# Kernel tuning notes

Measured on AMD Instinct MI355X. Metric: run time of the kernel, lower is better.

The kernel has to match this reference:

```python
import jax, jax.numpy as jnp
import numpy as np

SEQ, EMBED, H, QLR, KVLR, RD, VD = 4096, 2048, 16, 512, 512, 64, 128
KD = VD + RD  # full key/query head dim (content + rope)


def _make_rotary_pe(seq_len, dim):
    inv_freq = 1.0 / jnp.power(10000.0, jnp.arange(0, dim, 2) / dim)
    t = jnp.arange(seq_len)
    freqs = jnp.outer(t, inv_freq)  # (seq, dim//2)
    return jnp.sin(freqs), jnp.cos(freqs)


def _apply_rope(x, sin, cos):
    # x: (seq, ..., dim); sin/cos: (seq, dim//2)
    d = x.shape[-1] // 2
    x1, x2 = x[..., :d], x[..., d:]
    sin2 = jnp.concatenate([sin, sin], axis=-1)
    cos2 = jnp.concatenate([cos, cos], axis=-1)
    ne = x.ndim - 2
    sin2 = sin2.reshape(sin2.shape[0], *[1] * ne, sin2.shape[1])
    cos2 = cos2.reshape(cos2.shape[0], *[1] * ne, cos2.shape[1])
    rot = jnp.concatenate([-x2, x1], axis=-1)
    return x * cos2 + rot * sin2


def setup_inputs() -> dict:
    key = jax.random.key(0)
    ks = jax.random.split(key, 8)

    def w(k, out_dim, in_dim):
        return jax.random.normal(k, (out_dim, in_dim), dtype=jnp.float32) * (1.0 / np.sqrt(in_dim))

    x = jax.random.normal(ks[0], (SEQ, EMBED), dtype=jnp.float32)
    mask = jnp.tril(jnp.ones((SEQ, SEQ), dtype=bool))  # causal
    return {
        "x": x,
        "mask": mask,
        "w_q_down": w(ks[1], QLR, EMBED),
        "w_q_up": w(ks[2], H * VD, QLR),
        "w_q_rope": w(ks[3], H * RD, QLR),
        "w_kv_down": w(ks[4], KVLR, EMBED),
        "w_kv_up": w(ks[5], H * 2 * VD, KVLR),
        "w_k_rope": w(ks[6], RD, EMBED),
        "w_out": w(ks[7], EMBED, H * VD),
    }


def reference(x, mask, w_q_down, w_q_up, w_q_rope, w_kv_down, w_kv_up, w_k_rope, w_out):
    seq = x.shape[0]
    # query path through low-rank bottleneck
    c_q = x @ w_q_down.T                                   # (S, QLR)
    q_content = (c_q @ w_q_up.T).reshape(seq, H, VD)       # (S, H, VD)
    q_rope = (c_q @ w_q_rope.T).reshape(seq, H, RD)        # (S, H, RD)
    # kv path through shared low-rank bottleneck
    c_kv = x @ w_kv_down.T                                 # (S, KVLR)
    kv = c_kv @ w_kv_up.T                                  # (S, H*2*VD)
    k_content_flat, v_flat = jnp.split(kv, 2, axis=-1)
    k_content = k_content_flat.reshape(seq, H, VD)
    v = v_flat.reshape(seq, H, VD)
    # shared rope key (one per token, broadcast to heads)
    k_rope_shared = (x @ w_k_rope.T)[:, None, :]           # (S, 1, RD)
    sin, cos = _make_rotary_pe(seq, RD)
    q_rope_rot = _apply_rope(q_rope, sin, cos)             # (S, H, RD)
    k_rope_rot = jnp.tile(_apply_rope(k_rope_shared, sin, cos), (1, H, 1))
    q_final = jnp.concatenate([q_content, q_rope_rot], axis=-1)  # (S, H, KD)
    k_final = jnp.concatenate([k_content, k_rope_rot], axis=-1)  # (S, H, KD)
    # values zero-padded to key dim
    v_padded = jnp.concatenate(
        [v, jnp.zeros((seq, H, RD), dtype=v.dtype)], axis=-1)    # (S, H, KD)
    # scaled dot-product attention per head
    scale = 1.0 / jnp.sqrt(jnp.asarray(KD, dtype=x.dtype))
    scores = jnp.einsum("shd,thd->hst", q_final, k_final) * scale  # (H, S, S)
    scores = jnp.where(mask[None, :, :], scores, jnp.asarray(-1e9, dtype=scores.dtype))
    probs = jax.nn.softmax(scores, axis=-1)
    attn = jnp.einsum("hst,thd->shd", probs, v_padded)             # (S, H, KD)
    attn = attn[..., :VD].reshape(seq, H * VD)                     # drop zero-pad dims
    return attn @ w_out.T                                          # (S, EMBED)
```

## Files before the change

### kernel.cpp

```cpp
#include <hip/hip_runtime.h>


#define SEQ   4096
#define EMBED 2048
#define NHEAD 16
#define QLR   512
#define KVLR  512
#define RD    64
#define VD    128
#define KDIM  192

#define QSCALE 0.104121521f

typedef __attribute__((ext_vector_type(8)))  _Float16 half8;
typedef __attribute__((ext_vector_type(4)))  _Float16 half4;
typedef __attribute__((ext_vector_type(4)))  float    f32x4;
typedef __attribute__((ext_vector_type(16))) float    f32x16;
typedef __attribute__((ext_vector_type(2)))  unsigned int uint2v;
typedef __attribute__((ext_vector_type(4)))  unsigned int uint4v;

__device__ __forceinline__ void gload16(void* lds, const void* g) {
    __builtin_amdgcn_global_load_lds(
        (const __attribute__((address_space(1))) void*)g,
        (__attribute__((address_space(3))) void*)lds, 16, 0, 0);
}

__device__ __forceinline__ unsigned int pkh(float a, float b) {
    auto h = __builtin_amdgcn_cvt_pkrtz(a, b);
    return __builtin_bit_cast(unsigned int, h);
}

__global__ __launch_bounds__(256) void cvt_plain(const float* __restrict__ s,
                                                 _Float16* __restrict__ d, int n8) {
    const int i = blockIdx.x * 256 + threadIdx.x;
    if (i >= n8) return;
    const float4 a = reinterpret_cast<const float4*>(s)[i * 2];
    const float4 b = reinterpret_cast<const float4*>(s)[i * 2 + 1];
    half8 r;
    r[0] = (_Float16)a.x; r[1] = (_Float16)a.y; r[2] = (_Float16)a.z; r[3] = (_Float16)a.w;
    r[4] = (_Float16)b.x; r[5] = (_Float16)b.y; r[6] = (_Float16)b.z; r[7] = (_Float16)b.w;
    reinterpret_cast<half8*>(d)[i] = r;
}

__global__ __launch_bounds__(256) void cvt_down(const float* __restrict__ wqd,
                                                const float* __restrict__ wkvd,
                                                const float* __restrict__ wkr,
                                                _Float16* __restrict__ dst) {
    const int i = blockIdx.x * 256 + threadIdx.x;
    if (i >= 1152 * 2048 / 8) return;
    const int e = i * 8, row = e >> 11, col = e & 2047;
    const float* src = row < 512  ? wqd  + (size_t)row * 2048 + col
                     : row < 1024 ? wkvd + (size_t)(row - 512) * 2048 + col
                     : row < 1088 ? wkr  + (size_t)(row - 1024) * 2048 + col
                                  : nullptr;
    half8 r = {};
    if (src) {
        const float4 a = reinterpret_cast<const float4*>(src)[0];
        const float4 b = reinterpret_cast<const float4*>(src)[1];
        r[0] = (_Float16)a.x; r[1] = (_Float16)a.y; r[2] = (_Float16)a.z; r[3] = (_Float16)a.w;
        r[4] = (_Float16)b.x; r[5] = (_Float16)b.y; r[6] = (_Float16)b.z; r[7] = (_Float16)b.w;
    }
    reinterpret_cast<half8*>(dst)[i] = r;
}

__global__ __launch_bounds__(256) void cvt_qup(const float* __restrict__ wqu,
                                               const float* __restrict__ wqr,
                                               _Float16* __restrict__ dst) {
    const int i = blockIdx.x * 256 + threadIdx.x;
    if (i >= 3072 * 512 / 8) return;
    const int e = i * 8, row = e >> 9, col = e & 511;
    const float* src = row < 2048 ? wqu + (size_t)row * 512 + col
                                  : wqr + (size_t)(row - 2048) * 512 + col;
    const float4 a = reinterpret_cast<const float4*>(src)[0];
    const float4 b = reinterpret_cast<const float4*>(src)[1];
    half8 r;
    r[0] = (_Float16)a.x; r[1] = (_Float16)a.y; r[2] = (_Float16)a.z; r[3] = (_Float16)a.w;
    r[4] = (_Float16)b.x; r[5] = (_Float16)b.y; r[6] = (_Float16)b.z; r[7] = (_Float16)b.w;
    reinterpret_cast<half8*>(dst)[i] = r;
}

template <int EPI>
__global__ __launch_bounds__(256) void gemm_f16(const _Float16* __restrict__ A,
                                                const _Float16* __restrict__ B,
                                                _Float16* __restrict__ o0,
                                                _Float16* __restrict__ o1,
                                                _Float16* __restrict__ o2,
                                                float* __restrict__ of,
                                                int M, int N, int K)
{
    __shared__ _Float16 sA[128 * 64];
    __shared__ _Float16 sB[128 * 64];

    const int tid  = threadIdx.x;
    const int wid  = tid >> 6;
    const int lane = tid & 63;
    const int lr   = lane & 15;
    const int lg   = lane >> 4;
    const int row0 = blockIdx.y * 128;
    const int col0 = blockIdx.x * 128;
    const int war  = (wid >> 1) * 64;
    const int wac  = (wid & 1) * 64;

    const int sr = lane >> 3;
    const int sk = (lane & 7) * 8;
    const _Float16* Ab = A + (size_t)(row0 + wid * 8 + sr) * K + sk;
    const _Float16* Bb = B + (size_t)(col0 + wid * 8 + sr) * K + sk;

    f32x4 acc[4][4] = {};

    for (int k0 = 0; k0 < K; k0 += 64) {
#pragma unroll
        for (int i = 0; i < 4; ++i) {
            const int c = i * 4 + wid;
            gload16((char*)sA + c * 1024, Ab + (size_t)i * 32 * K + k0);
            gload16((char*)sB + c * 1024, Bb + (size_t)i * 32 * K + k0);
        }
        __syncthreads();

#pragma unroll
        for (int kk = 0; kk < 64; kk += 32) {
            half8 a[4], b[4];
#pragma unroll
            for (int i = 0; i < 4; ++i)
                a[i] = *reinterpret_cast<const half8*>(&sA[(war + i * 16 + lr) * 64 + kk + lg * 8]);
#pragma unroll
            for (int j = 0; j < 4; ++j)
                b[j] = *reinterpret_cast<const half8*>(&sB[(wac + j * 16 + lr) * 64 + kk + lg * 8]);
            __builtin_amdgcn_s_setprio(1);
#pragma unroll
            for (int i = 0; i < 4; ++i)
#pragma unroll
                for (int j = 0; j < 4; ++j)
                    acc[i][j] = __builtin_amdgcn_mfma_f32_16x16x32_f16(a[i], b[j], acc[i][j], 0, 0, 0);
            __builtin_amdgcn_s_setprio(0);
        }
        __syncthreads();
    }

#pragma unroll
    for (int i = 0; i < 4; ++i)
#pragma unroll
        for (int j = 0; j < 4; ++j) {
            const int grow0 = row0 + war + i * 16 + lg * 4;
            const int gcol  = col0 + wac + j * 16 + lr;
            if constexpr (EPI == 2) {
                if (gcol >= 2048) {
                    half4 pv;
#pragma unroll
                    for (int r = 0; r < 4; ++r) pv[r] = (_Float16)acc[i][j][r];
                    *reinterpret_cast<half4*>(&o1[(size_t)(gcol - 2048) * SEQ + grow0]) = pv;
                    continue;
                }
            }
#pragma unroll
            for (int r = 0; r < 4; ++r) {
                const int grow = grow0 + r;
                const float v = acc[i][j][r];
                if constexpr (EPI == 0) {
                    if (gcol < 512)       o0[(size_t)grow * 512 + gcol] = (_Float16)v;
                    else if (gcol < 1024) o1[(size_t)grow * 512 + gcol - 512] = (_Float16)v;
                    else if (gcol < 1088) o2[(size_t)grow * 64 + gcol - 1024] = (_Float16)v;
                } else if constexpr (EPI == 1) {
                    const float vs = v * QSCALE;
                    if (gcol < 2048)
                        o0[(size_t)grow * (NHEAD * KDIM) + (gcol >> 7) * KDIM + (gcol & 127)] = (_Float16)vs;
                    else {
                        const int c = gcol - 2048;
                        o0[(size_t)grow * (NHEAD * KDIM) + (c >> 6) * KDIM + VD + (c & 63)] = (_Float16)vs;
                    }
                } else if constexpr (EPI == 2) {
                    o0[((size_t)(gcol >> 7) * SEQ + grow) * KDIM + (gcol & 127)] = (_Float16)v;
                } else {
                    of[(size_t)grow * N + gcol] = v;
                }
            }
        }
}

__global__ __launch_bounds__(256) void rope_kernel(_Float16* __restrict__ qf,
                                                   _Float16* __restrict__ kf,
                                                   const _Float16* __restrict__ ktmp)
{
    __shared__ float s_sin[32], s_cos[32];
    const int s   = blockIdx.x;
    const int tid = threadIdx.x;
    if (tid < 32) {
        const double inv = exp(-(double)tid * (log(10000.0) / 32.0));
        const double ang = (double)s * inv;
        s_sin[tid] = (float)sin(ang);
        s_cos[tid] = (float)cos(ang);
    }
    __syncthreads();

    for (int p = tid; p < NHEAD * 32; p += 256) {
        const int h = p >> 5, i = p & 31;
        const size_t base = (size_t)s * (NHEAD * KDIM) + h * KDIM + VD;
        const float x1 = (float)qf[base + i];
        const float x2 = (float)qf[base + 32 + i];
        const float cs = s_cos[i], sn = s_sin[i];
        qf[base + i]      = (_Float16)(x1 * cs - x2 * sn);
        qf[base + 32 + i] = (_Float16)(x2 * cs + x1 * sn);
    }
    if (tid < 32) {
        const int i = tid;
        const float x1 = (float)ktmp[(size_t)s * RD + i];
        const float x2 = (float)ktmp[(size_t)s * RD + 32 + i];
        const float cs = s_cos[i], sn = s_sin[i];
        const _Float16 r1 = (_Float16)(x1 * cs - x2 * sn);
        const _Float16 r2 = (_Float16)(x2 * cs + x1 * sn);
#pragma unroll
        for (int h = 0; h < NHEAD; ++h) {
            const size_t base = ((size_t)h * SEQ + s) * KDIM + VD;
            kf[base + i]      = r1;
            kf[base + 32 + i] = r2;
        }
    }
}

__global__ __launch_bounds__(256, 2) void fattn(const _Float16* __restrict__ qf,
                                                const _Float16* __restrict__ kf,
                                                const _Float16* __restrict__ vT,
                                                _Float16* __restrict__ attn)
{
    __shared__ _Float16 sK[2][64 * 192];
    __shared__ _Float16 sV[2][128 * 64];

    const int idx = blockIdx.x;
    const int h   = idx & 15;
    const int qt  = 31 - (idx >> 4);
    const int q0  = qt * 128;

    const int tid  = threadIdx.x;
    const int wid  = tid >> 6;
    const int lane = tid & 63;
    const int l31  = lane & 31;
    const int h5   = lane >> 5;
    const int x7   = l31 & 7;
    const int qg   = q0 + wid * 32 + l31;
    const int q0w  = q0 + wid * 32;

    const _Float16* ksrc[6];
    int klds[6];
#pragma unroll
    for (int i = 0; i < 6; ++i) {
        const int c   = wid * 6 + i;
        const int gi  = c * 64 + lane;
        const int row = gi / 24;
        const int g   = gi % 24;
        ksrc[i] = kf + ((size_t)h * SEQ + row) * KDIM + ((g ^ (row & 7)) << 3);
        klds[i] = c * 1024;
    }
    const _Float16* vsrc[4];
    int vlds[4];
#pragma unroll
    for (int i = 0; i < 4; ++i) {
        const int c = wid * 4 + i;
        const int d = c * 8 + (lane >> 3);
        vsrc[i] = vT + ((size_t)h * VD + d) * SEQ + (((lane & 7) ^ (lane >> 3)) << 3);
        vlds[i] = c * 1024;
    }

    half8 qfr[12];
    {
        const _Float16* qb_ = qf + (size_t)qg * (NHEAD * KDIM) + h * KDIM + h5 * 8;
#pragma unroll
        for (int ks = 0; ks < 12; ++ks)
            qfr[ks] = *reinterpret_cast<const half8*>(qb_ + ks * 16);
    }

    f32x16 o0 = {}, o1 = {}, o2 = {}, o3 = {};
    float m_ = -1e30f, l_ = 0.0f;

    const int nt = 2 * qt + 2;

#pragma unroll
    for (int i = 0; i < 6; ++i) gload16((char*)sK[0] + klds[i], ksrc[i]);
#pragma unroll
    for (int i = 0; i < 4; ++i) gload16((char*)sV[0] + vlds[i], vsrc[i]);
    __syncthreads();

    int cur = 0;
    for (int t = 0; t < nt; ++t) {
        const int j0 = t * 64;

        if (t + 1 < nt) {
            const size_t joff = (size_t)(j0 + 64) * KDIM;
#pragma unroll
            for (int i = 0; i < 6; ++i)
                gload16((char*)sK[cur ^ 1] + klds[i], ksrc[i] + joff);
#pragma unroll
            for (int i = 0; i < 4; ++i)
                gload16((char*)sV[cur ^ 1] + vlds[i], vsrc[i] + j0 + 64);
        }

        f32x16 s0 = {}, s1 = {};
        {
            const char* kb = (const char*)sK[cur];
            __builtin_amdgcn_s_setprio(1);
#pragma unroll
            for (int ks = 0; ks < 12; ++ks) {
                const int go = ((ks * 2 + h5) ^ x7) << 4;
                const half8 ka = *reinterpret_cast<const half8*>(kb + l31 * 384 + go);
                const half8 kc = *reinterpret_cast<const half8*>(kb + (32 + l31) * 384 + go);
                s0 = __builtin_amdgcn_mfma_f32_32x32x16_f16(ka, qfr[ks], s0, 0, 0, 0);
                s1 = __builtin_amdgcn_mfma_f32_32x32x16_f16(kc, qfr[ks], s1, 0, 0, 0);
            }
            __builtin_amdgcn_s_setprio(0);
        }

        if (j0 + 63 > q0w) {
#pragma unroll
            for (int m = 0; m < 16; ++m) {
                const int kv = j0 + (m & 3) + 8 * (m >> 2) + 4 * h5;
                if (kv > qg)      s0[m] = -3.0e38f;
                if (kv + 32 > qg) s1[m] = -3.0e38f;
            }
        }

        float ma = fmaxf(s0[0], s0[1]);
        float mb = fmaxf(s1[0], s1[1]);
#pragma unroll
        for (int m = 2; m < 16; m += 2) {
            ma = fmaxf(fmaxf(ma, s0[m]), s0[m + 1]);
            mb = fmaxf(fmaxf(mb, s1[m]), s1[m + 1]);
        }
        float mx = fmaxf(ma, mb);
        mx = fmaxf(mx, __shfl_xor(mx, 32, 64));

        if (!__all(mx - m_ <= 11.5f)) {
            const float mn = fmaxf(m_, mx);
            const float alpha = exp2f(m_ - mn);
            m_ = mn;
            l_ *= alpha;
#pragma unroll
            for (int m = 0; m < 16; ++m) {
                o0[m] *= alpha; o1[m] *= alpha; o2[m] *= alpha; o3[m] *= alpha;
            }
        }
        float ra = 0.0f, rb = 0.0f, rc = 0.0f, rd = 0.0f;
#pragma unroll
        for (int m = 0; m < 16; m += 2) {
            const float pa = exp2f(s0[m] - m_);     s0[m] = pa;     ra += pa;
            const float pc = exp2f(s0[m + 1] - m_); s0[m + 1] = pc; rb += pc;
            const float pe = exp2f(s1[m] - m_);     s1[m] = pe;     rc += pe;
            const float pg = exp2f(s1[m + 1] - m_); s1[m + 1] = pg; rd += pg;
        }
        float rs = (ra + rb) + (rc + rd);
        rs += __shfl_xor(rs, 32, 64);
        l_ += rs;

        half8 pb0, pb1, pb2, pb3;
        {
            unsigned int x, x2, y, y2;
            x  = pkh(s0[0], s0[1]);  x2 = pkh(s0[2], s0[3]);
            y  = pkh(s0[4], s0[5]);  y2 = pkh(s0[6], s0[7]);
            uint2v r1 = __builtin_amdgcn_permlane32_swap(x, y, false, false);
            uint2v r2 = __builtin_amdgcn_permlane32_swap(x2, y2, false, false);
            { uint4v u = { r1[0], r2[0], r1[1], r2[1] }; pb0 = __builtin_bit_cast(half8, u); }
            x  = pkh(s0[8], s0[9]);  x2 = pkh(s0[10], s0[11]);
            y  = pkh(s0[12], s0[13]); y2 = pkh(s0[14], s0[15]);
            r1 = __builtin_amdgcn_permlane32_swap(x, y, false, false);
            r2 = __builtin_amdgcn_permlane32_swap(x2, y2, false, false);
            { uint4v u = { r1[0], r2[0], r1[1], r2[1] }; pb1 = __builtin_bit_cast(half8, u); }
            x  = pkh(s1[0], s1[1]);  x2 = pkh(s1[2], s1[3]);
            y  = pkh(s1[4], s1[5]);  y2 = pkh(s1[6], s1[7]);
            r1 = __builtin_amdgcn_permlane32_swap(x, y, false, false);
            r2 = __builtin_amdgcn_permlane32_swap(x2, y2, false, false);
            { uint4v u = { r1[0], r2[0], r1[1], r2[1] }; pb2 = __builtin_bit_cast(half8, u); }
            x  = pkh(s1[8], s1[9]);  x2 = pkh(s1[10], s1[11]);
            y  = pkh(s1[12], s1[13]); y2 = pkh(s1[14], s1[15]);
            r1 = __builtin_amdgcn_permlane32_swap(x, y, false, false);
            r2 = __builtin_amdgcn_permlane32_swap(x2, y2, false, false);
            { uint4v u = { r1[0], r2[0], r1[1], r2[1] }; pb3 = __builtin_bit_cast(half8, u); }
        }

        {
            const char* vbse = (const char*)sV[cur];
            __builtin_amdgcn_s_setprio(1);
#pragma unroll
            for (int ks = 0; ks < 4; ++ks) {
                const int go = ((ks * 2 + h5) ^ x7) << 4;
                const half8 pbk = ks == 0 ? pb0 : ks == 1 ? pb1 : ks == 2 ? pb2 : pb3;
                const half8 v0 = *reinterpret_cast<const half8*>(vbse + (l31)      * 128 + go);
                const half8 v1 = *reinterpret_cast<const half8*>(vbse + (32 + l31) * 128 + go);
                const half8 v2 = *reinterpret_cast<const half8*>(vbse + (64 + l31) * 128 + go);
                const half8 v3 = *reinterpret_cast<const half8*>(vbse + (96 + l31) * 128 + go);
                o0 = __builtin_amdgcn_mfma_f32_32x32x16_f16(v0, pbk, o0, 0, 0, 0);
                o1 = __builtin_amdgcn_mfma_f32_32x32x16_f16(v1, pbk, o1, 0, 0, 0);
                o2 = __builtin_amdgcn_mfma_f32_32x32x16_f16(v2, pbk, o2, 0, 0, 0);
                o3 = __builtin_amdgcn_mfma_f32_32x32x16_f16(v3, pbk, o3, 0, 0, 0);
            }
            __builtin_amdgcn_s_setprio(0);
        }

        __syncthreads();
        cur ^= 1;
    }

    const float invl = 1.0f / l_;
    _Float16* ob = attn + (size_t)qg * (NHEAD * VD) + h * VD + 4 * h5;
#pragma unroll
    for (int g = 0; g < 4; ++g) {
#pragma unroll
        for (int pp = 0; pp < 2; ++pp) {
            const int m = g * 4 + pp * 2;
            const int dof = pp * 2 + 8 * g;
            *reinterpret_cast<unsigned int*>(ob + dof) =
                pkh(o0[m] * invl, o0[m + 1] * invl);
            *reinterpret_cast<unsigned int*>(ob + 32 + dof) =
                pkh(o1[m] * invl, o1[m + 1] * invl);
            *reinterpret_cast<unsigned int*>(ob + 64 + dof) =
                pkh(o2[m] * invl, o2[m + 1] * invl);
            *reinterpret_cast<unsigned int*>(ob + 96 + dof) =
                pkh(o3[m] * invl, o3[m + 1] * invl);
        }
    }
}

extern "C" void kernel_launch(void* const* d_in, const int* in_sizes, int n_in,
                              void* d_out, int out_size, void* d_ws, size_t ws_size,
                              hipStream_t stream)
{
    (void)in_sizes; (void)n_in; (void)out_size; (void)ws_size;
    const float* x    = (const float*)d_in[0];
    const float* wqd  = (const float*)d_in[2];
    const float* wqu  = (const float*)d_in[3];
    const float* wqr  = (const float*)d_in[4];
    const float* wkvd = (const float*)d_in[5];
    const float* wkvu = (const float*)d_in[6];
    const float* wkr  = (const float*)d_in[7];
    const float* wout = (const float*)d_in[8];
    float* out = (float*)d_out;

    char* ws = (char*)d_ws;
    _Float16* x_h    = (_Float16*)ws; ws += (size_t)SEQ * EMBED * 2;
    _Float16* wdownh = (_Float16*)ws; ws += (size_t)1152 * EMBED * 2;
    _Float16* wquph  = (_Float16*)ws; ws += (size_t)3072 * QLR * 2;
    _Float16* wkvuh  = (_Float16*)ws; ws += (size_t)4096 * KVLR * 2;
    _Float16* c_q    = (_Float16*)ws; ws += (size_t)SEQ * QLR * 2;
    _Float16* c_kv   = (_Float16*)ws; ws += (size_t)SEQ * KVLR * 2;
    _Float16* ktmp   = (_Float16*)ws; ws += (size_t)SEQ * RD * 2;
    _Float16* qfin   = (_Float16*)ws; ws += (size_t)SEQ * NHEAD * KDIM * 2;
    _Float16* kfin   = (_Float16*)ws; ws += (size_t)SEQ * NHEAD * KDIM * 2;
    _Float16* vT     = (_Float16*)ws; ws += (size_t)NHEAD * VD * SEQ * 2;
    _Float16* attn   = x_h;
    _Float16* wouth  = c_q;

    dim3 blk(256);

    cvt_plain<<<dim3(4096), blk, 0, stream>>>(x, x_h, SEQ * EMBED / 8);
    cvt_down <<<dim3(1152), blk, 0, stream>>>(wqd, wkvd, wkr, wdownh);
    cvt_qup  <<<dim3(768),  blk, 0, stream>>>(wqu, wqr, wquph);
    cvt_plain<<<dim3(1024), blk, 0, stream>>>(wkvu, wkvuh, 4096 * KVLR / 8);

    gemm_f16<0><<<dim3(9, 32), blk, 0, stream>>>(
        x_h, wdownh, c_q, c_kv, ktmp, nullptr, SEQ, 1152, EMBED);
    gemm_f16<1><<<dim3(24, 32), blk, 0, stream>>>(
        c_q, wquph, qfin, nullptr, nullptr, nullptr, SEQ, 3072, QLR);
    gemm_f16<2><<<dim3(32, 32), blk, 0, stream>>>(
        c_kv, wkvuh, kfin, vT, nullptr, nullptr, SEQ, 4096, KVLR);

    cvt_plain<<<dim3(2048), blk, 0, stream>>>(wout, wouth, EMBED * EMBED / 8);

    rope_kernel<<<dim3(SEQ), blk, 0, stream>>>(qfin, kfin, ktmp);
    fattn<<<dim3(512), blk, 0, stream>>>(qfin, kfin, vT, attn);
    gemm_f16<3><<<dim3(16, 32), blk, 0, stream>>>(
        attn, wouth, nullptr, nullptr, nullptr, out, SEQ, EMBED, NHEAD * VD);
}
```

Baseline: 346.9 us.

## Give each attention wave two query sub-tiles to reuse K/V fragments

```diff
diff --git a/kernel.cpp b/kernel.cpp
--- a/kernel.cpp
+++ b/kernel.cpp
@@ -28,6 +28,14 @@
 __device__ __forceinline__ unsigned int pkh(float a, float b) {
     auto h = __builtin_amdgcn_cvt_pkrtz(a, b);
     return __builtin_bit_cast(unsigned int, h);
+}
+
+__device__ __forceinline__ float fexp2(float x) {
+#if __has_builtin(__builtin_amdgcn_exp2f)
+    return __builtin_amdgcn_exp2f(x);
+#else
+    return exp2f(x);
+#endif
 }
 
 __global__ __launch_bounds__(256) void cvt_plain(const float* __restrict__ s,
@@ -217,188 +225,82 @@
     }
 }
 
-__global__ __launch_bounds__(256, 2) void fattn(const _Float16* __restrict__ qf,
-                                                const _Float16* __restrict__ kf,
-                                                const _Float16* __restrict__ vT,
-                                                _Float16* __restrict__ attn)
+__device__ __forceinline__ void sm_pack(f32x16& s0, f32x16& s1,
+                                        f32x16& o0, f32x16& o1,
+                                        f32x16& o2, f32x16& o3,
+                                        float& m_, float& l_,
+                                        int j0, int qg, int q0base, int h5,
+                                        half8& pb0, half8& pb1,
+                                        half8& pb2, half8& pb3)
 {
-    __shared__ _Float16 sK[2][64 * 192];
-    __shared__ _Float16 sV[2][128 * 64];
-
-    const int idx = blockIdx.x;
-    const int h   = idx & 15;
-    const int qt  = 31 - (idx >> 4);
-    const int q0  = qt * 128;
-
-    const int tid  = threadIdx.x;
-    const int wid  = tid >> 6;
-    const int lane = tid & 63;
-    const int l31  = lane & 31;
-    const int h5   = lane >> 5;
-    const int x7   = l31 & 7;
-    const int qg   = q0 + wid * 32 + l31;
-    const int q0w  = q0 + wid * 32;
-
-    const _Float16* ksrc[6];
-    int klds[6];
-#pragma unroll
-    for (int i = 0; i < 6; ++i) {
-        const int c   = wid * 6 + i;
-        const int gi  = c * 64 + lane;
-        const int row = gi / 24;
-        const int g   = gi % 24;
-        ksrc[i] = kf + ((size_t)h * SEQ + row) * KDIM + ((g ^ (row & 7)) << 3);
-        klds[i] = c * 1024;
-    }
-    const _Float16* vsrc[4];
-    int vlds[4];
-#pragma unroll
-    for (int i = 0; i < 4; ++i) {
-        const int c = wid * 4 + i;
-        const int d = c * 8 + (lane >> 3);
-        vsrc[i] = vT + ((size_t)h * VD + d) * SEQ + (((lane & 7) ^ (lane >> 3)) << 3);
-        vlds[i] = c * 1024;
-    }
-
-    half8 qfr[12];
-    {
-        const _Float16* qb_ = qf + (size_t)qg * (NHEAD * KDIM) + h * KDIM + h5 * 8;
-#pragma unroll
-        for (int ks = 0; ks < 12; ++ks)
-            qfr[ks] = *reinterpret_cast<const half8*>(qb_ + ks * 16);
-    }
-
-    f32x16 o0 = {}, o1 = {}, o2 = {}, o3 = {};
-    float m_ = -1e30f, l_ = 0.0f;
-
-    const int nt = 2 * qt + 2;
-
-#pragma unroll
-    for (int i = 0; i < 6; ++i) gload16((char*)sK[0] + klds[i], ksrc[i]);
-#pragma unroll
-    for (int i = 0; i < 4; ++i) gload16((char*)sV[0] + vlds[i], vsrc[i]);
-    __syncthreads();
-
-    int cur = 0;
-    for (int t = 0; t < nt; ++t) {
-        const int j0 = t * 64;
-
-        if (t + 1 < nt) {
-            const size_t joff = (size_t)(j0 + 64) * KDIM;
-#pragma unroll
-            for (int i = 0; i < 6; ++i)
-                gload16((char*)sK[cur ^ 1] + klds[i], ksrc[i] + joff);
-#pragma unroll
-            for (int i = 0; i < 4; ++i)
-                gload16((char*)sV[cur ^ 1] + vlds[i], vsrc[i] + j0 + 64);
-        }
-
-        f32x16 s0 = {}, s1 = {};
-        {
-            const char* kb = (const char*)sK[cur];
-            __builtin_amdgcn_s_setprio(1);
-#pragma unroll
-            for (int ks = 0; ks < 12; ++ks) {
-                const int go = ((ks * 2 + h5) ^ x7) << 4;
-                const half8 ka = *reinterpret_cast<const half8*>(kb + l31 * 384 + go);
-                const half8 kc = *reinterpret_cast<const half8*>(kb + (32 + l31) * 384 + go);
-                s0 = __builtin_amdgcn_mfma_f32_32x32x16_f16(ka, qfr[ks], s0, 0, 0, 0);
-                s1 = __builtin_amdgcn_mfma_f32_32x32x16_f16(kc, qfr[ks], s1, 0, 0, 0);
-            }
-            __builtin_amdgcn_s_setprio(0);
-        }
-
-        if (j0 + 63 > q0w) {
-#pragma unroll
-            for (int m = 0; m < 16; ++m) {
-                const int kv = j0 + (m & 3) + 8 * (m >> 2) + 4 * h5;
-                if (kv > qg)      s0[m] = -3.0e38f;
-                if (kv + 32 > qg) s1[m] = -3.0e38f;
-            }
-        }
-
-        float ma = fmaxf(s0[0], s0[1]);
-        float mb = fmaxf(s1[0], s1[1]);
-#pragma unroll
-        for (int m = 2; m < 16; m += 2) {
-            ma = fmaxf(fmaxf(ma, s0[m]), s0[m + 1]);
-            mb = fmaxf(fmaxf(mb, s1[m]), s1[m + 1]);
-        }
-        float mx = fmaxf(ma, mb);
-        mx = fmaxf(mx, __shfl_xor(mx, 32, 64));
-
-        if (!__all(mx - m_ <= 11.5f)) {
-            const float mn = fmaxf(m_, mx);
-            const float alpha = exp2f(m_ - mn);
-            m_ = mn;
-            l_ *= alpha;
-#pragma unroll
-            for (int m = 0; m < 16; ++m) {
-                o0[m] *= alpha; o1[m] *= alpha; o2[m] *= alpha; o3[m] *= alpha;
-            }
-        }
-        float ra = 0.0f, rb = 0.0f, rc = 0.0f, rd = 0.0f;
-#pragma unroll
-        for (int m = 0; m < 16; m += 2) {
-            const float pa = exp2f(s0[m] - m_);     s0[m] = pa;     ra += pa;
-            const float pc = exp2f(s0[m + 1] - m_); s0[m + 1] = pc; rb += pc;
-            const float pe = exp2f(s1[m] - m_);     s1[m] = pe;     rc += pe;
-            const float pg = exp2f(s1[m + 1] - m_); s1[m + 1] = pg; rd += pg;
-        }
-        float rs = (ra + rb) + (rc + rd);
-        rs += __shfl_xor(rs, 32, 64);
-        l_ += rs;
-
-        half8 pb0, pb1, pb2, pb3;
-        {
-            unsigned int x, x2, y, y2;
-            x  = pkh(s0[0], s0[1]);  x2 = pkh(s0[2], s0[3]);
-            y  = pkh(s0[4], s0[5]);  y2 = pkh(s0[6], s0[7]);
-            uint2v r1 = __builtin_amdgcn_permlane32_swap(x, y, false, false);
-            uint2v r2 = __builtin_amdgcn_permlane32_swap(x2, y2, false, false);
-            { uint4v u = { r1[0], r2[0], r1[1], r2[1] }; pb0 = __builtin_bit_cast(half8, u); }
-            x  = pkh(s0[8], s0[9]);  x2 = pkh(s0[10], s0[11]);
-            y  = pkh(s0[12], s0[13]); y2 = pkh(s0[14], s0[15]);
-            r1 = __builtin_amdgcn_permlane32_swap(x, y, false, false);
-            r2 = __builtin_amdgcn_permlane32_swap(x2, y2, false, false);
-            { uint4v u = { r1[0], r2[0], r1[1], r2[1] }; pb1 = __builtin_bit_cast(half8, u); }
-            x  = pkh(s1[0], s1[1]);  x2 = pkh(s1[2], s1[3]);
-            y  = pkh(s1[4], s1[5]);  y2 = pkh(s1[6], s1[7]);
-            r1 = __builtin_amdgcn_permlane32_swap(x, y, false, false);
-            r2 = __builtin_amdgcn_permlane32_swap(x2, y2, false, false);
-            { uint4v u = { r1[0], r2[0], r1[1], r2[1] }; pb2 = __builtin_bit_cast(half8, u); }
-            x  = pkh(s1[8], s1[9]);  x2 = pkh(s1[10], s1[11]);
-            y  = pkh(s1[12], s1[13]); y2 = pkh(s1[14], s1[15]);
-            r1 = __builtin_amdgcn_permlane32_swap(x, y, false, false);
-            r2 = __builtin_amdgcn_permlane32_swap(x2, y2, false, false);
-            { uint4v u = { r1[0], r2[0], r1[1], r2[1] }; pb3 = __builtin_bit_cast(half8, u); }
-        }
-
-        {
-            const char* vbse = (const char*)sV[cur];
-            __builtin_amdgcn_s_setprio(1);
-#pragma unroll
-            for (int ks = 0; ks < 4; ++ks) {
-                const int go = ((ks * 2 + h5) ^ x7) << 4;
-                const half8 pbk = ks == 0 ? pb0 : ks == 1 ? pb1 : ks == 2 ? pb2 : pb3;
-                const half8 v0 = *reinterpret_cast<const half8*>(vbse + (l31)      * 128 + go);
-                const half8 v1 = *reinterpret_cast<const half8*>(vbse + (32 + l31) * 128 + go);
-                const half8 v2 = *reinterpret_cast<const half8*>(vbse + (64 + l31) * 128 + go);
-                const half8 v3 = *reinterpret_cast<const half8*>(vbse + (96 + l31) * 128 + go);
-                o0 = __builtin_amdgcn_mfma_f32_32x32x16_f16(v0, pbk, o0, 0, 0, 0);
-                o1 = __builtin_amdgcn_mfma_f32_32x32x16_f16(v1, pbk, o1, 0, 0, 0);
-                o2 = __builtin_amdgcn_mfma_f32_32x32x16_f16(v2, pbk, o2, 0, 0, 0);
-                o3 = __builtin_amdgcn_mfma_f32_32x32x16_f16(v3, pbk, o3, 0, 0, 0);
-            }
-            __builtin_amdgcn_s_setprio(0);
-        }
-
-        __syncthreads();
-        cur ^= 1;
-    }
-
+    if (j0 + 63 > q0base) {
+#pragma unroll
+        for (int m = 0; m < 16; ++m) {
+            const int kv = j0 + (m & 3) + 8 * (m >> 2) + 4 * h5;
+            if (kv > qg)      s0[m] = -3.0e38f;
+            if (kv + 32 > qg) s1[m] = -3.0e38f;
+        }
+    }
+    float ma = fmaxf(s0[0], s0[1]);
+    float mb = fmaxf(s1[0], s1[1]);
+#pragma unroll
+    for (int m = 2; m < 16; m += 2) {
+        ma = fmaxf(fmaxf(ma, s0[m]), s0[m + 1]);
+        mb = fmaxf(fmaxf(mb, s1[m]), s1[m + 1]);
+    }
+    float mx = fmaxf(ma, mb);
+    mx = fmaxf(mx, __shfl_xor(mx, 32, 64));
+
+    if (!__all(mx - m_ <= 11.5f)) {
+        const float mn = fmaxf(m_, mx);
+        const float alpha = fexp2(m_ - mn);
+        m_ = mn;
+        l_ *= alpha;
+#pragma unroll
+        for (int m = 0; m < 16; ++m) {
+            o0[m] *= alpha; o1[m] *= alpha; o2[m] *= alpha; o3[m] *= alpha;
+        }
+    }
+    float ra = 0.0f, rb = 0.0f, rc = 0.0f, rd = 0.0f;
+#pragma unroll
+    for (int m = 0; m < 16; m += 2) {
+        const float pa = fexp2(s0[m] - m_);     s0[m] = pa;     ra += pa;
+        const float pc = fexp2(s0[m + 1] - m_); s0[m + 1] = pc; rb += pc;
+        const float pe = fexp2(s1[m] - m_);     s1[m] = pe;     rc += pe;
+        const float pg = fexp2(s1[m + 1] - m_); s1[m + 1] = pg; rd += pg;
+    }
+    float rs = (ra + rb) + (rc + rd);
+    rs += __shfl_xor(rs, 32, 64);
+    l_ += rs;
+
+    unsigned int x, x2, y, y2;
+    x  = pkh(s0[0], s0[1]);  x2 = pkh(s0[2], s0[3]);
+    y  = pkh(s0[4], s0[5]);  y2 = pkh(s0[6], s0[7]);
+    uint2v r1 = __builtin_amdgcn_permlane32_swap(x, y, false, false);
+    uint2v r2 = __builtin_amdgcn_permlane32_swap(x2, y2, false, false);
+    { uint4v u = { r1[0], r2[0], r1[1], r2[1] }; pb0 = __builtin_bit_cast(half8, u); }
+    x  = pkh(s0[8], s0[9]);   x2 = pkh(s0[10], s0[11]);
+    y  = pkh(s0[12], s0[13]); y2 = pkh(s0[14], s0[15]);
+    r1 = __builtin_amdgcn_permlane32_swap(x, y, false, false);
+    r2 = __builtin_amdgcn_permlane32_swap(x2, y2, false, false);
+    { uint4v u = { r1[0], r2[0], r1[1], r2[1] }; pb1 = __builtin_bit_cast(half8, u); }
+    x  = pkh(s1[0], s1[1]);  x2 = pkh(s1[2], s1[3]);
+    y  = pkh(s1[4], s1[5]);  y2 = pkh(s1[6], s1[7]);
+    r1 = __builtin_amdgcn_permlane32_swap(x, y, false, false);
+    r2 = __builtin_amdgcn_permlane32_swap(x2, y2, false, false);
+    { uint4v u = { r1[0], r2[0], r1[1], r2[1] }; pb2 = __builtin_bit_cast(half8, u); }
+    x  = pkh(s1[8], s1[9]);   x2 = pkh(s1[10], s1[11]);
+    y  = pkh(s1[12], s1[13]); y2 = pkh(s1[14], s1[15]);
+    r1 = __builtin_amdgcn_permlane32_swap(x, y, false, false);
+    r2 = __builtin_amdgcn_permlane32_swap(x2, y2, false, false);
+    { uint4v u = { r1[0], r2[0], r1[1], r2[1] }; pb3 = __builtin_bit_cast(half8, u); }
+}
+
+__device__ __forceinline__ void store_o(f32x16& o0, f32x16& o1,
+                                        f32x16& o2, f32x16& o3,
+                                        float l_, _Float16* ob)
+{
     const float invl = 1.0f / l_;
-    _Float16* ob = attn + (size_t)qg * (NHEAD * VD) + h * VD + 4 * h5;
 #pragma unroll
     for (int g = 0; g < 4; ++g) {
 #pragma unroll
@@ -415,6 +317,145 @@
                 pkh(o3[m] * invl, o3[m + 1] * invl);
         }
     }
+}
+
+__global__ __launch_bounds__(128, 1) void fattn(const _Float16* __restrict__ qf,
+                                                const _Float16* __restrict__ kf,
+                                                const _Float16* __restrict__ vT,
+                                                _Float16* __restrict__ attn)
+{
+    __shared__ _Float16 sK[2][64 * 192];
+    __shared__ _Float16 sV[2][128 * 64];
+
+    const int idx = blockIdx.x;
+    const int h   = idx & 15;
+    const int j   = idx >> 4;
+    const int qt  = (j < 16) ? (31 - 2 * j) : (2 * (j - 16));
+    const int q0  = qt * 128;
+
+    const int tid  = threadIdx.x;
+    const int wid  = tid >> 6;
+    const int lane = tid & 63;
+    const int l31  = lane & 31;
+    const int h5   = lane >> 5;
+    const int x7   = l31 & 7;
+    const int q0w  = q0 + wid * 64;
+    const int qgA  = q0w + l31;
+    const int qgB  = q0w + 32 + l31;
+
+    const _Float16* ksrc[12];
+    int klds[12];
+#pragma unroll
+    for (int i = 0; i < 12; ++i) {
+        const int c   = wid * 12 + i;
+        const int gi  = c * 64 + lane;
+        const int row = gi / 24;
+        const int g   = gi % 24;
+        ksrc[i] = kf + ((size_t)h * SEQ + row) * KDIM + ((g ^ (row & 7)) << 3);
+        klds[i] = c * 1024;
+    }
+    const _Float16* vsrc[8];
+    int vlds[8];
+#pragma unroll
+    for (int i = 0; i < 8; ++i) {
+        const int c = wid * 8 + i;
+        const int d = c * 8 + (lane >> 3);
+        vsrc[i] = vT + ((size_t)h * VD + d) * SEQ + (((lane & 7) ^ (lane >> 3)) << 3);
+        vlds[i] = c * 1024;
+    }
+
+    half8 qA[12], qB[12];
+    {
+        const _Float16* qa_ = qf + (size_t)qgA * (NHEAD * KDIM) + h * KDIM + h5 * 8;
+        const _Float16* qb_ = qf + (size_t)qgB * (NHEAD * KDIM) + h * KDIM + h5 * 8;
+#pragma unroll
+        for (int ks = 0; ks < 12; ++ks) {
+            qA[ks] = *reinterpret_cast<const half8*>(qa_ + ks * 16);
+            qB[ks] = *reinterpret_cast<const half8*>(qb_ + ks * 16);
+        }
+    }
+
+    f32x16 oA0 = {}, oA1 = {}, oA2 = {}, oA3 = {};
+    f32x16 oB0 = {}, oB1 = {}, oB2 = {}, oB3 = {};
+    float mA = -1e30f, lA = 0.0f, mB = -1e30f, lB = 0.0f;
+
+    const int nt = 2 * qt + 2;
+
+#pragma unroll
+    for (int i = 0; i < 12; ++i) gload16((char*)sK[0] + klds[i], ksrc[i]);
+#pragma unroll
+    for (int i = 0; i < 8; ++i)  gload16((char*)sV[0] + vlds[i], vsrc[i]);
+    __syncthreads();
+
+    int cur = 0;
+    for (int t = 0; t < nt; ++t) {
+        const int j0 = t * 64;
+
+        if (t + 1 < nt) {
+            const size_t joff = (size_t)(j0 + 64) * KDIM;
+#pragma unroll
+            for (int i = 0; i < 12; ++i)
+                gload16((char*)sK[cur ^ 1] + klds[i], ksrc[i] + joff);
+#pragma unroll
+            for (int i = 0; i < 8; ++i)
+                gload16((char*)sV[cur ^ 1] + vlds[i], vsrc[i] + j0 + 64);
+        }
+
+        f32x16 sA0 = {}, sA1 = {}, sB0 = {}, sB1 = {};
+        {
+            const char* kb = (const char*)sK[cur];
+            __builtin_amdgcn_s_setprio(1);
+#pragma unroll
+            for (int ks = 0; ks < 12; ++ks) {
+                const int go = ((ks * 2 + h5) ^ x7) << 4;
+                const half8 ka = *reinterpret_cast<const half8*>(kb + l31 * 384 + go);
+                const half8 kc = *reinterpret_cast<const half8*>(kb + (32 + l31) * 384 + go);
+                sA0 = __builtin_amdgcn_mfma_f32_32x32x16_f16(ka, qA[ks], sA0, 0, 0, 0);
+                sB0 = __builtin_amdgcn_mfma_f32_32x32x16_f16(ka, qB[ks], sB0, 0, 0, 0);
+                sA1 = __builtin_amdgcn_mfma_f32_32x32x16_f16(kc, qA[ks], sA1, 0, 0, 0);
+                sB1 = __builtin_amdgcn_mfma_f32_32x32x16_f16(kc, qB[ks], sB1, 0, 0, 0);
+            }
+            __builtin_amdgcn_s_setprio(0);
+        }
+
+        half8 pA0, pA1, pA2, pA3, pB0, pB1, pB2, pB3;
+        sm_pack(sA0, sA1, oA0, oA1, oA2, oA3, mA, lA, j0, qgA, q0w,      h5,
+                pA0, pA1, pA2, pA3);
+        sm_pack(sB0, sB1, oB0, oB1, oB2, oB3, mB, lB, j0, qgB, q0w + 32, h5,
+                pB0, pB1, pB2, pB3);
+
+        {
+            const char* vbse = (const char*)sV[cur];
+            __builtin_amdgcn_s_setprio(1);
+#pragma unroll
+            for (int ks = 0; ks < 4; ++ks) {
+                const int go = ((ks * 2 + h5) ^ x7) << 4;
+                const half8 pA = ks == 0 ? pA0 : ks == 1 ? pA1 : ks == 2 ? pA2 : pA3;
+                const half8 pB = ks == 0 ? pB0 : ks == 1 ? pB1 : ks == 2 ? pB2 : pB3;
+                const half8 v0 = *reinterpret_cast<const half8*>(vbse + (l31)      * 128 + go);
+                const half8 v1 = *reinterpret_cast<const half8*>(vbse + (32 + l31) * 128 + go);
+                const half8 v2 = *reinterpret_cast<const half8*>(vbse + (64 + l31) * 128 + go);
+                const half8 v3 = *reinterpret_cast<const half8*>(vbse + (96 + l31) * 128 + go);
+                oA0 = __builtin_amdgcn_mfma_f32_32x32x16_f16(v0, pA, oA0, 0, 0, 0);
+                oB0 = __builtin_amdgcn_mfma_f32_32x32x16_f16(v0, pB, oB0, 0, 0, 0);
+                oA1 = __builtin_amdgcn_mfma_f32_32x32x16_f16(v1, pA, oA1, 0, 0, 0);
+                oB1 = __builtin_amdgcn_mfma_f32_32x32x16_f16(v1, pB, oB1, 0, 0, 0);
+                oA2 = __builtin_amdgcn_mfma_f32_32x32x16_f16(v2, pA, oA2, 0, 0, 0);
+                oB2 = __builtin_amdgcn_mfma_f32_32x32x16_f16(v2, pB, oB2, 0, 0, 0);
+                oA3 = __builtin_amdgcn_mfma_f32_32x32x16_f16(v3, pA, oA3, 0, 0, 0);
+                oB3 = __builtin_amdgcn_mfma_f32_32x32x16_f16(v3, pB, oB3, 0, 0, 0);
+            }
+            __builtin_amdgcn_s_setprio(0);
+        }
+
+        __syncthreads();
+        cur ^= 1;
+    }
+
+    store_o(oA0, oA1, oA2, oA3, lA,
+            attn + (size_t)qgA * (NHEAD * VD) + h * VD + 4 * h5);
+    store_o(oB0, oB1, oB2, oB3, lB,
+            attn + (size_t)qgB * (NHEAD * VD) + h * VD + 4 * h5);
 }
 
 extern "C" void kernel_launch(void* const* d_in, const int* in_sizes, int n_in,
@@ -463,7 +504,7 @@
     cvt_plain<<<dim3(2048), blk, 0, stream>>>(wout, wouth, EMBED * EMBED / 8);
 
     rope_kernel<<<dim3(SEQ), blk, 0, stream>>>(qfin, kfin, ktmp);
-    fattn<<<dim3(512), blk, 0, stream>>>(qfin, kfin, vT, attn);
+    fattn<<<dim3(512), dim3(128), 0, stream>>>(qfin, kfin, vT, attn);
     gemm_f16<3><<<dim3(16, 32), blk, 0, stream>>>(
         attn, wouth, nullptr, nullptr, nullptr, out, SEQ, EMBED, NHEAD * VD);
 }
```

After: 704.3 us. +103.0%, slower.
